# Optimization experiments

Hardware: AMD Instinct MI355X
Metric: run time of the kernel (lower is better)

The kernel has to match this reference:

```python
import math
import jax, jax.numpy as jnp
import numpy as np

L = 16
LOG2T = 19
T = 1 << LOG2T
F = 2
N_MIN = 16
N_MAX = 2048
N_PTS = 1048576

# intended geometric growth factor (source has a parenthesization bug)
_B = math.exp((math.log(N_MAX) - math.log(N_MIN)) / (L - 1))
RESOLUTIONS = [int(math.floor(N_MIN * (_B ** i))) for i in range(L)]

# 8 corner offsets of a voxel, [8, 3]
_OFFS_NP = np.stack(np.meshgrid([0, 1], [0, 1], [0, 1], indexing='ij'), -1).reshape(8, 3)
# spatial hash primes from Instant-NGP
_PRIMES_NP = np.array([1, 2654435761, 805459861], dtype=np.uint32)


def setup_inputs() -> dict:
    key = jax.random.key(0)
    k1, k2 = jax.random.split(key)
    x = jax.random.uniform(k1, (N_PTS, 3), dtype=jnp.float32)  # positions in [0,1)
    table = jax.random.normal(k2, (L, T, F), dtype=jnp.float32) * 1e-4
    return {"x": x, "table": table}


def _encode(x, table):
    offs_i = jnp.asarray(_OFFS_NP, dtype=jnp.uint32)          # [8,3]
    offs_f = jnp.asarray(_OFFS_NP, dtype=x.dtype)             # [8,3]
    primes = jnp.asarray(_PRIMES_NP)                          # [3] uint32
    mask = jnp.uint32(T - 1)
    outs = []
    for lvl in range(L):
        res = RESOLUTIONS[lvl]
        xs = x * res                                           # [N,3]
        x0 = jnp.floor(xs)
        w = xs - x0                                            # [N,3] trilerp weights
        # corner integer coords, [N,8,3]
        c = x0.astype(jnp.uint32)[:, None, :] + offs_i[None]
        # spatial hash: xor of coord*prime, masked to T (T is a power of 2)
        hp = c * primes                                        # uint32 wraparound mul
        h = (hp[..., 0] ^ hp[..., 1] ^ hp[..., 2]) & mask      # [N,8]
        feats = table[lvl][h.astype(jnp.int32)]                # [N,8,F] gather
        # trilinear weights: prod over dims of (w if corner==1 else 1-w)
        wts = jnp.prod(jnp.where(offs_f[None] == 1.0, w[:, None, :], 1.0 - w[:, None, :]), axis=-1)  # [N,8]
        outs.append(jnp.einsum('nc,ncf->nf', wts, feats))      # [N,F]
    return jnp.concatenate(outs, axis=-1)                      # [N, L*F]


def reference(x, table):
    return _encode(x, table)
```

## Files before the change

kernel.cpp:

```cpp
#include <hip/hip_runtime.h>
#include <cmath>

#define NPTS   1048576
#define NLVL   16
#define NLOW   5
#define T      (1u << 19)
#define TMASK  (T - 1u)
#define P1     2654435761u
#define P2     805459861u

typedef float    v2f __attribute__((ext_vector_type(2)));
typedef float    v4f __attribute__((ext_vector_type(4)));
typedef _Float16 v2h __attribute__((ext_vector_type(2)));
typedef _Float16 v4h __attribute__((ext_vector_type(4)));

struct Corners { uint32_t h[8]; float wt[8]; };

__device__ __forceinline__ Corners mk_corners(float px, float py, float pz, float rf) {
    Corners cc;
    const float xs0 = px * rf, xs1 = py * rf, xs2 = pz * rf;
    const float f0 = floorf(xs0), f1 = floorf(xs1), f2 = floorf(xs2);
    const float w0 = xs0 - f0, w1 = xs1 - f1, w2 = xs2 - f2;
    const uint32_t i0 = (uint32_t)f0, i1 = (uint32_t)f1, i2 = (uint32_t)f2;
    const uint32_t A0 = i0,      A1 = i0 + 1u;
    const uint32_t B0 = i1 * P1, B1 = B0 + P1;
    const uint32_t C0 = i2 * P2, C1 = C0 + P2;
    cc.h[0] = (A0 ^ B0 ^ C0) & TMASK;  cc.h[1] = (A0 ^ B0 ^ C1) & TMASK;
    cc.h[2] = (A0 ^ B1 ^ C0) & TMASK;  cc.h[3] = (A0 ^ B1 ^ C1) & TMASK;
    cc.h[4] = (A1 ^ B0 ^ C0) & TMASK;  cc.h[5] = (A1 ^ B0 ^ C1) & TMASK;
    cc.h[6] = (A1 ^ B1 ^ C0) & TMASK;  cc.h[7] = (A1 ^ B1 ^ C1) & TMASK;
    const float u0 = 1.0f - w0, u1 = 1.0f - w1, u2 = 1.0f - w2;
    cc.wt[0] = (u0 * u1) * u2;  cc.wt[1] = (u0 * u1) * w2;
    cc.wt[2] = (u0 * w1) * u2;  cc.wt[3] = (u0 * w1) * w2;
    cc.wt[4] = (w0 * u1) * u2;  cc.wt[5] = (w0 * u1) * w2;
    cc.wt[6] = (w0 * w1) * u2;  cc.wt[7] = (w0 * w1) * w2;
    return cc;
}

__global__ __launch_bounds__(256) void hashgrid_lvl2pt(
    const float* __restrict__ x,
    const float* __restrict__ tb,
    _Float16* __restrict__ wsl,
    float rf)
{
    const int t = blockIdx.x * 256 + threadIdx.x;

    const v2f q0 = __builtin_nontemporal_load((const v2f*)(x + 6 * (size_t)t + 0));
    const v2f q1 = __builtin_nontemporal_load((const v2f*)(x + 6 * (size_t)t + 2));
    const v2f q2 = __builtin_nontemporal_load((const v2f*)(x + 6 * (size_t)t + 4));

    const Corners c0 = mk_corners(q0.x, q0.y, q1.x, rf);
    const Corners c1 = mk_corners(q1.y, q2.x, q2.y, rf);

    float a00 = 0.f, a01 = 0.f, a10 = 0.f, a11 = 0.f;
#pragma unroll
    for (int c = 0; c < 8; ++c) {
        const float2 g0 = *(const float2*)(tb + 2 * (size_t)c0.h[c]);
        const float2 g1 = *(const float2*)(tb + 2 * (size_t)c1.h[c]);
        a00 += c0.wt[c] * g0.x;  a01 += c0.wt[c] * g0.y;
        a10 += c1.wt[c] * g1.x;  a11 += c1.wt[c] * g1.y;
    }
    v4h r;
    r.x = (_Float16)a00;  r.y = (_Float16)a01;
    r.z = (_Float16)a10;  r.w = (_Float16)a11;
    __builtin_nontemporal_store(r, (v4h*)(wsl + 4 * (size_t)t));
}

__global__ __launch_bounds__(256) void hashgrid_lvl1(
    const float* __restrict__ x,
    const float* __restrict__ tb,
    _Float16* __restrict__ wsl,
    float rf)
{
    const int n = blockIdx.x * 256 + threadIdx.x;
    const float px = __builtin_nontemporal_load(x + 3 * (size_t)n + 0);
    const float py = __builtin_nontemporal_load(x + 3 * (size_t)n + 1);
    const float pz = __builtin_nontemporal_load(x + 3 * (size_t)n + 2);
    const Corners cc = mk_corners(px, py, pz, rf);
    float a0 = 0.f, a1 = 0.f;
#pragma unroll
    for (int c = 0; c < 8; ++c) {
        const float2 g = *(const float2*)(tb + 2 * (size_t)cc.h[c]);
        a0 += cc.wt[c] * g.x;
        a1 += cc.wt[c] * g.y;
    }
    v2h r; r.x = (_Float16)a0; r.y = (_Float16)a1;
    __builtin_nontemporal_store(r, (v2h*)(wsl + 2 * (size_t)n));
}

__global__ __launch_bounds__(256) void hashgrid_transpose(
    const _Float16* __restrict__ ws,
    float* __restrict__ out)
{
    const int n = blockIdx.x * 256 + threadIdx.x;
    float acc[2 * NLVL];
#pragma unroll
    for (int l = 0; l < NLVL; ++l) {
        const v2h g = __builtin_nontemporal_load(
            (const v2h*)(ws + ((size_t)l << 21) + (size_t)n * 2));
        acc[2 * l + 0] = (float)g.x;
        acc[2 * l + 1] = (float)g.y;
    }
    v4f* op = (v4f*)(out + (size_t)n * 32);
#pragma unroll
    for (int k = 0; k < 8; ++k) {
        v4f v; v.x = acc[4*k]; v.y = acc[4*k+1]; v.z = acc[4*k+2]; v.w = acc[4*k+3];
        op[k] = v;
    }
}

__global__ __launch_bounds__(256) void hashgrid_lvl_direct(
    const float* __restrict__ x,
    const float* __restrict__ tb,
    float* __restrict__ outl,
    float rf)
{
    const int n = blockIdx.x * 256 + threadIdx.x;
    const float px = __builtin_nontemporal_load(x + 3 * (size_t)n + 0);
    const float py = __builtin_nontemporal_load(x + 3 * (size_t)n + 1);
    const float pz = __builtin_nontemporal_load(x + 3 * (size_t)n + 2);
    const Corners cc = mk_corners(px, py, pz, rf);
    float a0 = 0.f, a1 = 0.f;
#pragma unroll
    for (int c = 0; c < 8; ++c) {
        const float2 g = *(const float2*)(tb + 2 * (size_t)cc.h[c]);
        a0 += cc.wt[c] * g.x;
        a1 += cc.wt[c] * g.y;
    }
    outl[(size_t)n * 32 + 0] = a0;
    outl[(size_t)n * 32 + 1] = a1;
}

extern "C" void kernel_launch(void* const* d_in, const int* in_sizes, int n_in,
                              void* d_out, int out_size, void* d_ws, size_t ws_size,
                              hipStream_t stream) {
    const float* x     = (const float*)d_in[0];
    const float* table = (const float*)d_in[1];
    float* out         = (float*)d_out;
    _Float16* ws       = (_Float16*)d_ws;

    double (*volatile p_log)(double)          = log;
    double (*volatile p_exp)(double)          = exp;
    double (*volatile p_pow)(double, double)  = pow;
    double (*volatile p_floor)(double)        = floor;

    const double b = p_exp((p_log(2048.0) - p_log(16.0)) / 15.0);
    float rf[NLVL];
    for (int l = 0; l < NLVL; ++l)
        rf[l] = (float)(int)p_floor(16.0 * p_pow(b, (double)l));

    const bool use_ws = ws_size >= (size_t)NLVL * NPTS * 2 * sizeof(_Float16);

    if (!use_ws) {
        for (int l = 0; l < NLVL; ++l)
            hashgrid_lvl_direct<<<NPTS / 256, 256, 0, stream>>>(
                x, table + ((size_t)l << 20), out + 2 * l, rf[l]);
        return;
    }

    for (int l = NLOW; l < NLVL; ++l) {
        hashgrid_lvl2pt<<<NPTS / 512, 256, 0, stream>>>(
            x, table + ((size_t)l << 20), ws + ((size_t)l << 21), rf[l]);
    }
    for (int l = 0; l < NLOW; ++l) {
        hashgrid_lvl1<<<NPTS / 256, 256, 0, stream>>>(
            x, table + ((size_t)l << 20), ws + ((size_t)l << 21), rf[l]);
    }
    hashgrid_transpose<<<NPTS / 256, 256, 0, stream>>>(ws, out);
}
```

Before: 560.3 us.

## Merge per-level gather launches into one 2D-grid kernel with two-point transpose

Replaces the sixteen per-level kernel launches, which mixed one-point and two-point-per-thread variants, with a single launch over a 2D grid where blockIdx.y selects the level. Every level now processes two points per thread. The transpose kernel also reads 4 halfs per level and writes two output rows per thread. This removes launch gaps and tail effects between levels, and it lets blocks from different levels run concurrently. The cost is that the low levels lose their one-point-per-thread variant, and blocks now follow x-major order, which can change how well each level's table stays in cache.

```diff
diff --git a/kernel.cpp b/kernel.cpp
--- a/kernel.cpp
+++ b/kernel.cpp
@@ -3,7 +3,6 @@
 
 #define NPTS   1048576
 #define NLVL   16
-#define NLOW   5
 #define T      (1u << 19)
 #define TMASK  (T - 1u)
 #define P1     2654435761u
@@ -15,6 +14,7 @@
 typedef _Float16 v4h __attribute__((ext_vector_type(4)));
 
 struct Corners { uint32_t h[8]; float wt[8]; };
+struct RfArr   { float r[NLVL]; };
 
 __device__ __forceinline__ Corners mk_corners(float px, float py, float pz, float rf) {
     Corners cc;
@@ -37,12 +37,17 @@
     return cc;
 }
 
-__global__ __launch_bounds__(256) void hashgrid_lvl2pt(
+__global__ __launch_bounds__(256) void hashgrid_mega(
     const float* __restrict__ x,
-    const float* __restrict__ tb,
-    _Float16* __restrict__ wsl,
-    float rf)
+    const float* __restrict__ table,
+    _Float16* __restrict__ ws,
+    RfArr rfa)
 {
+    const int   lvl = blockIdx.y;
+    const float rf  = rfa.r[lvl];
+    const float* __restrict__ tb  = table + ((size_t)lvl << 20);
+    _Float16*  __restrict__   wsl = ws    + ((size_t)lvl << 21);
+
     const int t = blockIdx.x * 256 + threadIdx.x;
 
     const v2f q0 = __builtin_nontemporal_load((const v2f*)(x + 6 * (size_t)t + 0));
@@ -66,46 +71,32 @@
     __builtin_nontemporal_store(r, (v4h*)(wsl + 4 * (size_t)t));
 }
 
-__global__ __launch_bounds__(256) void hashgrid_lvl1(
-    const float* __restrict__ x,
-    const float* __restrict__ tb,
-    _Float16* __restrict__ wsl,
-    float rf)
-{
-    const int n = blockIdx.x * 256 + threadIdx.x;
-    const float px = __builtin_nontemporal_load(x + 3 * (size_t)n + 0);
-    const float py = __builtin_nontemporal_load(x + 3 * (size_t)n + 1);
-    const float pz = __builtin_nontemporal_load(x + 3 * (size_t)n + 2);
-    const Corners cc = mk_corners(px, py, pz, rf);
-    float a0 = 0.f, a1 = 0.f;
-#pragma unroll
-    for (int c = 0; c < 8; ++c) {
-        const float2 g = *(const float2*)(tb + 2 * (size_t)cc.h[c]);
-        a0 += cc.wt[c] * g.x;
-        a1 += cc.wt[c] * g.y;
-    }
-    v2h r; r.x = (_Float16)a0; r.y = (_Float16)a1;
-    __builtin_nontemporal_store(r, (v2h*)(wsl + 2 * (size_t)n));
-}
-
-__global__ __launch_bounds__(256) void hashgrid_transpose(
+__global__ __launch_bounds__(256) void hashgrid_transpose2(
     const _Float16* __restrict__ ws,
     float* __restrict__ out)
 {
-    const int n = blockIdx.x * 256 + threadIdx.x;
-    float acc[2 * NLVL];
+    const int t = blockIdx.x * 256 + threadIdx.x;
+    float acc0[2 * NLVL], acc1[2 * NLVL];
 #pragma unroll
     for (int l = 0; l < NLVL; ++l) {
-        const v2h g = __builtin_nontemporal_load(
-            (const v2h*)(ws + ((size_t)l << 21) + (size_t)n * 2));
-        acc[2 * l + 0] = (float)g.x;
-        acc[2 * l + 1] = (float)g.y;
+        const v4h g = __builtin_nontemporal_load(
+            (const v4h*)(ws + ((size_t)l << 21) + 4 * (size_t)t));
+        acc0[2 * l + 0] = (float)g.x;
+        acc0[2 * l + 1] = (float)g.y;
+        acc1[2 * l + 0] = (float)g.z;
+        acc1[2 * l + 1] = (float)g.w;
     }
-    v4f* op = (v4f*)(out + (size_t)n * 32);
+    v4f* o0 = (v4f*)(out + (size_t)(2 * t) * 32);
+    v4f* o1 = (v4f*)(out + (size_t)(2 * t + 1) * 32);
 #pragma unroll
     for (int k = 0; k < 8; ++k) {
-        v4f v; v.x = acc[4*k]; v.y = acc[4*k+1]; v.z = acc[4*k+2]; v.w = acc[4*k+3];
-        op[k] = v;
+        v4f v0; v0.x = acc0[4*k]; v0.y = acc0[4*k+1]; v0.z = acc0[4*k+2]; v0.w = acc0[4*k+3];
+        o0[k] = v0;
+    }
+#pragma unroll
+    for (int k = 0; k < 8; ++k) {
+        v4f v1; v1.x = acc1[4*k]; v1.y = acc1[4*k+1]; v1.z = acc1[4*k+2]; v1.w = acc1[4*k+3];
+        o1[k] = v1;
     }
 }
 
@@ -145,26 +136,20 @@
     double (*volatile p_floor)(double)        = floor;
 
     const double b = p_exp((p_log(2048.0) - p_log(16.0)) / 15.0);
-    float rf[NLVL];
+    RfArr rfa;
     for (int l = 0; l < NLVL; ++l)
-        rf[l] = (float)(int)p_floor(16.0 * p_pow(b, (double)l));
+        rfa.r[l] = (float)(int)p_floor(16.0 * p_pow(b, (double)l));
 
     const bool use_ws = ws_size >= (size_t)NLVL * NPTS * 2 * sizeof(_Float16);
 
     if (!use_ws) {
         for (int l = 0; l < NLVL; ++l)
             hashgrid_lvl_direct<<<NPTS / 256, 256, 0, stream>>>(
-                x, table + ((size_t)l << 20), out + 2 * l, rf[l]);
+                x, table + ((size_t)l << 20), out + 2 * l, rfa.r[l]);
         return;
     }
 
-    for (int l = NLOW; l < NLVL; ++l) {
-        hashgrid_lvl2pt<<<NPTS / 512, 256, 0, stream>>>(
-            x, table + ((size_t)l << 20), ws + ((size_t)l << 21), rf[l]);
-    }
-    for (int l = 0; l < NLOW; ++l) {
-        hashgrid_lvl1<<<NPTS / 256, 256, 0, stream>>>(
-            x, table + ((size_t)l << 20), ws + ((size_t)l << 21), rf[l]);
-    }
-    hashgrid_transpose<<<NPTS / 256, 256, 0, stream>>>(ws, out);
+    dim3 grid(NPTS / 512, NLVL);
+    hashgrid_mega<<<grid, 256, 0, stream>>>(x, table, ws, rfa);
+    hashgrid_transpose2<<<NPTS / 512, 256, 0, stream>>>(ws, out);
 }
```

Result: slower. 612.3 us (+9.3%).
